# Optimization experiments

Measured on AMD Instinct MI355X. Metric: run time of the kernel, lower is better.

The kernel has to match this reference:

```python
import jax, jax.numpy as jnp
import numpy as np

B, S, D, H = 2, 2048, 1024, 16
DK = D // H
NEG = -1000000000.0


def setup_inputs() -> dict:
    key = jax.random.key(0)
    ks = jax.random.split(key, 12)
    s = 1.0 / np.sqrt(D)
    return {
        "Q": jax.random.normal(ks[0], (B, S, D), jnp.float32),
        "K": jax.random.normal(ks[1], (B, S, D), jnp.float32),
        "V": jax.random.normal(ks[2], (B, S, D), jnp.float32),
        "attn_mask": jnp.zeros((B, S, S), jnp.bool_),
        "WQ_w": jax.random.normal(ks[3], (D, D), jnp.float32) * s,
        "WQ_b": jnp.zeros((D,), jnp.float32),
        "WK_w": jax.random.normal(ks[4], (D, D), jnp.float32) * s,
        "WK_b": jnp.zeros((D,), jnp.float32),
        "WV_w": jax.random.normal(ks[5], (D, D), jnp.float32) * s,
        "WV_b": jnp.zeros((D,), jnp.float32),
        "fc_w": jax.random.normal(ks[6], (D, D), jnp.float32) * s,
        "fc_b": jnp.zeros((D,), jnp.float32),
    }


def reference(Q, K, V, attn_mask, WQ_w, WQ_b, WK_w, WK_b, WV_w, WV_b, fc_w, fc_b):
    b = Q.shape[0]
    # linear projections (torch Linear: x @ W^T + b), split heads -> [b, h, s, dk]
    q = (Q @ WQ_w.T + WQ_b).reshape(b, -1, H, DK).transpose(0, 2, 1, 3)
    k = (K @ WK_w.T + WK_b).reshape(b, -1, H, DK).transpose(0, 2, 1, 3)
    v = (V @ WV_w.T + WV_b).reshape(b, -1, H, DK).transpose(0, 2, 1, 3)
    # scaled dot-product attention with masked_fill
    scores = jnp.einsum("bhqd,bhkd->bhqk", q, k) / jnp.sqrt(jnp.float32(DK))
    scores = jnp.where(attn_mask[:, None, :, :], NEG, scores)
    attn_weights = jax.nn.softmax(scores, axis=-1)  # dropout p=0 -> identity
    attn = jnp.einsum("bhqk,bhkd->bhqd", attn_weights, v)
    attn = attn.transpose(0, 2, 1, 3).reshape(b, -1, H * DK)
    output = attn @ fc_w.T + fc_b
    return output, attn_weights
```

## Files before the change

### kernel.cpp

```cpp
#include <hip/hip_runtime.h>
#include <cstdint>
#include <cstddef>

constexpr int CB = 2;
constexpr int CS = 2048;
constexpr int CD = 1024;
constexpr int CH = 16;
constexpr int CDK = 64;
constexpr float NEGV = -1000000000.0f;

typedef __bf16 bf16x8 __attribute__((ext_vector_type(8)));
typedef float f32x4 __attribute__((ext_vector_type(4)));
typedef unsigned short u16x8 __attribute__((ext_vector_type(8)));
typedef unsigned short u16x4 __attribute__((ext_vector_type(4)));

static __device__ __forceinline__ unsigned short f2bf(float x) {
  unsigned int u = __float_as_uint(x);
  u += 0x7fffu + ((u >> 16) & 1u);
  return (unsigned short)(u >> 16);
}
static __device__ __forceinline__ bf16x8 bc8(u16x8 u) {
  return __builtin_bit_cast(bf16x8, u);
}
static __device__ __forceinline__ f32x4 mfma16(bf16x8 a, bf16x8 b, f32x4 c) {
  return __builtin_amdgcn_mfma_f32_16x16x32_bf16(a, b, c, 0, 0, 0);
}

struct CvtArgs {
  const float* src[7];
  unsigned short* dst[7];
  int n4[7];
};

__global__ __launch_bounds__(256) void cvt_all(CvtArgs a) {
  const int r = blockIdx.y;
  const float* __restrict__ in = a.src[r];
  unsigned short* __restrict__ out = a.dst[r];
  const int n4 = a.n4[r];
  const int stride = gridDim.x * 256;
  for (int i = blockIdx.x * 256 + threadIdx.x; i < n4; i += stride) {
    float4 v = reinterpret_cast<const float4*>(in)[i];
    u16x4 o;
    o[0] = f2bf(v.x); o[1] = f2bf(v.y); o[2] = f2bf(v.z); o[3] = f2bf(v.w);
    reinterpret_cast<u16x4*>(out)[i] = o;
  }
}

constexpr int GBM = 128, GBN = 64, GBK = 32, GLD = 40;

template <int MODE>
__global__ __launch_bounds__(256) void gemm_nt(const unsigned short* __restrict__ X,
                                               const unsigned short* __restrict__ Wt,
                                               const float* __restrict__ bias,
                                               void* __restrict__ outp,
                                               int M, int N, int K, float oscale) {
  __shared__ unsigned short lA[GBM * GLD];
  __shared__ unsigned short lB[GBN * GLD];
  const int tid = threadIdx.x, lane = tid & 63, wid = tid >> 6;
  const int mbase = blockIdx.y * GBM, nbase = blockIdx.x * GBN;
  const int wm = (wid & 1) * 64, wn = (wid >> 1) * 32;
  const int trow = tid >> 2, tcol = (tid & 3) * 8;

  f32x4 acc[4][2] = {};

  for (int k0 = 0; k0 < K; k0 += GBK) {
    __syncthreads();
    *reinterpret_cast<u16x8*>(&lA[trow * GLD + tcol]) =
        *reinterpret_cast<const u16x8*>(&X[(size_t)(mbase + trow) * K + k0 + tcol]);
    *reinterpret_cast<u16x8*>(&lA[(trow + 64) * GLD + tcol]) =
        *reinterpret_cast<const u16x8*>(&X[(size_t)(mbase + trow + 64) * K + k0 + tcol]);
    *reinterpret_cast<u16x8*>(&lB[trow * GLD + tcol]) =
        *reinterpret_cast<const u16x8*>(&Wt[(size_t)(nbase + trow) * K + k0 + tcol]);
    __syncthreads();

    bf16x8 af[4], bfv[2];
#pragma unroll
    for (int i = 0; i < 4; ++i)
      af[i] = bc8(*reinterpret_cast<const u16x8*>(
          &lA[(wm + i * 16 + (lane & 15)) * GLD + (lane >> 4) * 8]));
#pragma unroll
    for (int j = 0; j < 2; ++j)
      bfv[j] = bc8(*reinterpret_cast<const u16x8*>(
          &lB[(wn + j * 16 + (lane & 15)) * GLD + (lane >> 4) * 8]));
#pragma unroll
    for (int i = 0; i < 4; ++i)
#pragma unroll
      for (int j = 0; j < 2; ++j)
        acc[i][j] = mfma16(af[i], bfv[j], acc[i][j]);
  }

#pragma unroll
  for (int j = 0; j < 2; ++j) {
    const int colb = nbase + wn + j * 16 + (lane & 15);
    const float bv = bias[colb];
#pragma unroll
    for (int i = 0; i < 4; ++i) {
#pragma unroll
      for (int r = 0; r < 4; ++r) {
        const int rowb = mbase + wm + i * 16 + (lane >> 4) * 4 + r;
        const float v = (acc[i][j][r] + bv) * oscale;
        if constexpr (MODE == 2) {
          reinterpret_cast<float*>(outp)[(size_t)rowb * N + colb] = v;
        } else {
          const int bb = rowb >> 11, sr = rowb & (CS - 1);
          const int hh = colb >> 6, dk = colb & (CDK - 1);
          if constexpr (MODE == 0)
            reinterpret_cast<unsigned short*>(outp)[(((size_t)bb * CH + hh) * CS + sr) * CDK + dk] =
                f2bf(v);
          else
            reinterpret_cast<unsigned short*>(outp)[(((size_t)bb * CH + hh) * CDK + dk) * CS + sr] =
                f2bf(v);
        }
      }
    }
  }
}

constexpr int WLD = 68;

__global__ __launch_bounds__(256, 4) void attn_fused(const unsigned short* __restrict__ qh,
                                                     const unsigned short* __restrict__ kh,
                                                     const unsigned short* __restrict__ vT,
                                                     const unsigned char* __restrict__ mask,
                                                     float* __restrict__ attnw,
                                                     unsigned short* __restrict__ attn_pre) {
  __shared__ unsigned short lK[2][64 * 64];
  __shared__ float lW[4][16 * WLD];

  const int tid = threadIdx.x, lane = tid & 63, wid = tid >> 6;
  const int bid = blockIdx.x;
  const int swz = (bid & 7) * 128 + (bid >> 3);
  const int qt = swz & 31, hh = (swz >> 5) & 15, b = swz >> 9;
  const int bh = b * CH + hh;
  const int qw = qt * 64 + wid * 16;
  const int fr = lane & 15, fc = lane >> 4;

  const unsigned short* qp = qh + ((size_t)bh * CS + qw + fr) * CDK + fc * 8;
  const bf16x8 aq0 = bc8(*reinterpret_cast<const u16x8*>(qp));
  const bf16x8 aq1 = bc8(*reinterpret_cast<const u16x8*>(qp + 32));

  const char* ktile0 = (const char*)(kh + (size_t)bh * CS * CDK);
  const unsigned char* mrow = mask + ((size_t)b * CS + qw + (lane >> 2)) * CS + (lane & 3) * 16;

  auto stage = [&](int buf, int kt) {
    const char* src = ktile0 + (size_t)kt * 8192;
#pragma unroll
    for (int cc = 0; cc < 2; ++cc) {
      const int ob = (wid * 2 + cc) * 1024;
      const int o = ob + lane * 16;
      const int so = o ^ (((o >> 7) & 7) << 4);
      __builtin_amdgcn_global_load_lds(
          (const __attribute__((address_space(1))) void*)(src + so),
          (__attribute__((address_space(3))) void*)((char*)(&lK[buf][0]) + ob), 16, 0, 0);
    }
  };
  auto kfr = [&](int buf, int g, int half) -> bf16x8 {
    const int row = g * 16 + fr;
    const int slot = (fc + half * 4) ^ (row & 7);
    return bc8(*reinterpret_cast<const u16x8*>(&lK[buf][row * 64 + slot * 8]));
  };

  float l_r[4] = {0.f, 0.f, 0.f, 0.f};
  unsigned int dirtybits = 0;

  stage(0, 0);
  __syncthreads();
  for (int kt = 0; kt < CS / 64; ++kt) {
    if (kt < CS / 64 - 1) stage((kt + 1) & 1, kt + 1);
    const uint4 mv = *reinterpret_cast<const uint4*>(mrow + kt * 64);
    const int nz = (mv.x | mv.y | mv.z | mv.w) != 0;
    const int dirty = __ballot(nz) != 0ull;
    const int buf = kt & 1;

    f32x4 sf[4];
#pragma unroll
    for (int g = 0; g < 4; ++g) {
      f32x4 a = {0.f, 0.f, 0.f, 0.f};
      a = mfma16(aq0, kfr(buf, g, 0), a);
      a = mfma16(aq1, kfr(buf, g, 1), a);
      sf[g] = a;
    }
    if (dirty) {
      dirtybits |= (1u << kt);
#pragma unroll
      for (int g = 0; g < 4; ++g)
#pragma unroll
        for (int r = 0; r < 4; ++r) {
          const unsigned char mb =
              mask[((size_t)b * CS + qw + fc * 4 + r) * CS + kt * 64 + g * 16 + fr];
          if (mb) sf[g][r] = NEGV;
        }
    }
#pragma unroll
    for (int r = 0; r < 4; ++r)
      l_r[r] += __expf(sf[0][r]) + __expf(sf[1][r]) + __expf(sf[2][r]) + __expf(sf[3][r]);
    __syncthreads();
  }

  float linv[4];
#pragma unroll
  for (int r = 0; r < 4; ++r) {
    float s = l_r[r];
    s += __shfl_xor(s, 1);
    s += __shfl_xor(s, 2);
    s += __shfl_xor(s, 4);
    s += __shfl_xor(s, 8);
    linv[r] = 1.0f / s;
  }

  const unsigned short* vfrag = vT + ((size_t)bh * CDK + fr) * CS + fc * 8;

  f32x4 o[4] = {};
  stage(0, 0);
  __syncthreads();
  for (int kt = 0; kt < CS / 64; ++kt) {
    if (kt < CS / 64 - 1) stage((kt + 1) & 1, kt + 1);
    const int buf = kt & 1;

    u16x8 vr[8];
#pragma unroll
    for (int g = 0; g < 4; ++g) {
      const unsigned short* vp = vfrag + (size_t)g * 16 * CS + kt * 64;
      vr[2 * g] = *reinterpret_cast<const u16x8*>(vp);
      vr[2 * g + 1] = *reinterpret_cast<const u16x8*>(vp + 32);
    }

    f32x4 sf[4];
#pragma unroll
    for (int g = 0; g < 4; ++g) {
      f32x4 a = {0.f, 0.f, 0.f, 0.f};
      a = mfma16(aq0, kfr(buf, g, 0), a);
      a = mfma16(aq1, kfr(buf, g, 1), a);
      sf[g] = a;
    }
    if ((dirtybits >> kt) & 1u) {
#pragma unroll
      for (int g = 0; g < 4; ++g)
#pragma unroll
        for (int r = 0; r < 4; ++r) {
          const unsigned char mb =
              mask[((size_t)b * CS + qw + fc * 4 + r) * CS + kt * 64 + g * 16 + fr];
          if (mb) sf[g][r] = NEGV;
        }
    }
#pragma unroll
    for (int g = 0; g < 4; ++g)
#pragma unroll
      for (int r = 0; r < 4; ++r) sf[g][r] = __expf(sf[g][r]) * linv[r];

#pragma unroll
    for (int g = 0; g < 4; ++g)
#pragma unroll
      for (int r = 0; r < 4; ++r)
        lW[wid][(fc * 4 + r) * WLD + g * 16 + fr] = sf[g][r];

#pragma unroll
    for (int it = 0; it < 4; ++it) {
      const int row = it * 4 + fc;
      const f32x4 wv = *reinterpret_cast<const f32x4*>(&lW[wid][row * WLD + fr * 4]);
      __builtin_nontemporal_store(
          wv, reinterpret_cast<f32x4*>(
                  &attnw[((size_t)bh * CS + qw + row) * CS + kt * 64 + fr * 4]));
    }

    bf16x8 wa[2];
#pragma unroll
    for (int c = 0; c < 2; ++c) {
      const f32x4 t0 = *reinterpret_cast<const f32x4*>(&lW[wid][fr * WLD + c * 32 + fc * 8]);
      const f32x4 t1 = *reinterpret_cast<const f32x4*>(&lW[wid][fr * WLD + c * 32 + fc * 8 + 4]);
      u16x8 u;
#pragma unroll
      for (int z = 0; z < 4; ++z) { u[z] = f2bf(t0[z]); u[z + 4] = f2bf(t1[z]); }
      wa[c] = bc8(u);
    }
#pragma unroll
    for (int g = 0; g < 4; ++g) {
      o[g] = mfma16(wa[0], bc8(vr[2 * g]), o[g]);
      o[g] = mfma16(wa[1], bc8(vr[2 * g + 1]), o[g]);
    }
    __syncthreads();
  }

#pragma unroll
  for (int g = 0; g < 4; ++g)
#pragma unroll
    for (int r = 0; r < 4; ++r) {
      const int q = qw + fc * 4 + r;
      attn_pre[(((size_t)b * CS + q) * CH + hh) * CDK + g * 16 + fr] = f2bf(o[g][r]);
    }
}

extern "C" void kernel_launch(void* const* d_in, const int* in_sizes, int n_in,
                              void* d_out, int out_size, void* d_ws, size_t ws_size,
                              hipStream_t stream) {
  (void)in_sizes; (void)n_in; (void)out_size; (void)ws_size;

  const float* Qf = (const float*)d_in[0];
  const float* Kf = (const float*)d_in[1];
  const float* Vf = (const float*)d_in[2];
  const unsigned char* mask = (const unsigned char*)d_in[3];
  const float* WQw = (const float*)d_in[4];
  const float* WQb = (const float*)d_in[5];
  const float* WKw = (const float*)d_in[6];
  const float* WKb = (const float*)d_in[7];
  const float* WVw = (const float*)d_in[8];
  const float* WVb = (const float*)d_in[9];
  const float* fcw = (const float*)d_in[10];
  const float* fcb = (const float*)d_in[11];

  float* out0 = (float*)d_out;
  float* attnw = out0 + (size_t)CB * CS * CD;

  char* w = (char*)d_ws;
  unsigned short* Qb = (unsigned short*)(w);
  unsigned short* Kb = (unsigned short*)(w + 8388608);
  unsigned short* Vb = (unsigned short*)(w + 2 * 8388608);
  unsigned short* Wqb = (unsigned short*)(w + 3 * 8388608);
  unsigned short* Wkb = Wqb + 1048576;
  unsigned short* Wvb = Wkb + 1048576;
  unsigned short* Wfb = Wvb + 1048576;
  unsigned short* qhp = (unsigned short*)(w + 3 * 8388608 + 4 * 2097152);
  unsigned short* khp = qhp + 4194304;
  unsigned short* vTp = khp + 4194304;
  unsigned short* apre = Qb;

  const int NELEM4 = (CB * CS * CD) / 4;
  const int WELEM4 = (CD * CD) / 4;

  CvtArgs ca;
  ca.src[0] = Qf;  ca.dst[0] = Qb;  ca.n4[0] = NELEM4;
  ca.src[1] = Kf;  ca.dst[1] = Kb;  ca.n4[1] = NELEM4;
  ca.src[2] = Vf;  ca.dst[2] = Vb;  ca.n4[2] = NELEM4;
  ca.src[3] = WQw; ca.dst[3] = Wqb; ca.n4[3] = WELEM4;
  ca.src[4] = WKw; ca.dst[4] = Wkb; ca.n4[4] = WELEM4;
  ca.src[5] = WVw; ca.dst[5] = Wvb; ca.n4[5] = WELEM4;
  ca.src[6] = fcw; ca.dst[6] = Wfb; ca.n4[6] = WELEM4;
  cvt_all<<<dim3(512, 7), 256, 0, stream>>>(ca);

  dim3 gg(CD / GBN, (CB * CS) / GBM);
  gemm_nt<0><<<gg, 256, 0, stream>>>(Qb, Wqb, WQb, qhp, CB * CS, CD, CD, 0.125f);
  gemm_nt<0><<<gg, 256, 0, stream>>>(Kb, Wkb, WKb, khp, CB * CS, CD, CD, 1.0f);
  gemm_nt<1><<<gg, 256, 0, stream>>>(Vb, Wvb, WVb, vTp, CB * CS, CD, CD, 1.0f);

  attn_fused<<<dim3(1024), 256, 0, stream>>>(qhp, khp, vTp, mask, attnw, apre);

  gemm_nt<2><<<gg, 256, 0, stream>>>(apre, Wfb, fcb, out0, CB * CS, CD, CD, 1.0f);
}
```

Before: 293.0 us.

## Pre-swizzle K/V into MFMA fragment layout, batch QKV GEMMs, drop LDS staging

The QKV projections now run as one batched launch, and the GEMM body uses async global-to-LDS loads with double buffering and an XOR swizzle. The K and V projections are written straight into a per-tile MFMA fragment layout, so the attention kernel loads K and V fragments directly into registers. This removes the K shared-memory staging and the per-tile barriers. The Q scale folds in log2(e) so softmax can use exp2f, mask dirtiness is precomputed in a prologue, and P is converted to bf16 with the packed cvt instruction. Occupancy hint drops to 3 blocks per SM, trading register pressure for the register-held K/V prefetch.

After: 257.2 us. 1.14x faster.

```diff
diff --git a/kernel.cpp b/kernel.cpp
--- a/kernel.cpp
+++ b/kernel.cpp
@@ -8,6 +8,7 @@
 constexpr int CH = 16;
 constexpr int CDK = 64;
 constexpr float NEGV = -1000000000.0f;
+constexpr float QSCALE = 0.18033688011112042f;
 
 typedef __bf16 bf16x8 __attribute__((ext_vector_type(8)));
 typedef float f32x4 __attribute__((ext_vector_type(4)));
@@ -46,85 +47,124 @@
   }
 }
 
-constexpr int GBM = 128, GBN = 64, GBK = 32, GLD = 40;
-
-template <int MODE>
-__global__ __launch_bounds__(256) void gemm_nt(const unsigned short* __restrict__ X,
+constexpr int GK = 1024, GNT = GK / 32;
+
+struct QKVArgs {
+  const unsigned short* X[3];
+  const unsigned short* W[3];
+  const float* bias[3];
+  unsigned short* out[3];
+  float osc[3];
+};
+
+template <typename EPI>
+__device__ __forceinline__ void gemm_body(const unsigned short* __restrict__ X,
+                                          const unsigned short* __restrict__ Wt,
+                                          EPI epi) {
+  __shared__ unsigned short lA[2][128 * 32];
+  __shared__ unsigned short lB[2][64 * 32];
+  const int tid = threadIdx.x, lane = tid & 63, wid = tid >> 6;
+  const int fr = lane & 15, fc = lane >> 4;
+  const int mbase = blockIdx.y * 128, nbase = blockIdx.x * 64;
+  const int wm = (wid & 1) * 64, wn = (wid >> 1) * 32;
+
+  const int srow = wid * 16 + (lane >> 2);
+  const int sslot = (lane & 3) ^ (srow & 3);
+  const unsigned short* a0 = X + (size_t)(mbase + srow) * GK + sslot * 8;
+  const unsigned short* b0 = Wt + (size_t)(nbase + srow) * GK + sslot * 8;
+
+  auto stage = [&](int buf, int k0) {
+    __builtin_amdgcn_global_load_lds(
+        (const __attribute__((address_space(1))) void*)(a0 + k0),
+        (__attribute__((address_space(3))) void*)((char*)&lA[buf][0] + wid * 1024), 16, 0, 0);
+    __builtin_amdgcn_global_load_lds(
+        (const __attribute__((address_space(1))) void*)(a0 + (size_t)64 * GK + k0),
+        (__attribute__((address_space(3))) void*)((char*)&lA[buf][0] + 4096 + wid * 1024), 16, 0, 0);
+    __builtin_amdgcn_global_load_lds(
+        (const __attribute__((address_space(1))) void*)(b0 + k0),
+        (__attribute__((address_space(3))) void*)((char*)&lB[buf][0] + wid * 1024), 16, 0, 0);
+  };
+
+  f32x4 acc[4][2] = {};
+  stage(0, 0);
+  __syncthreads();
+  for (int t = 0; t < GNT; ++t) {
+    if (t + 1 < GNT) stage((t + 1) & 1, (t + 1) * 32);
+    const int buf = t & 1;
+    bf16x8 af[4], bfv[2];
+#pragma unroll
+    for (int i = 0; i < 4; ++i) {
+      const int row = wm + i * 16 + fr;
+      af[i] = bc8(*reinterpret_cast<const u16x8*>(&lA[buf][row * 32 + ((fc ^ (row & 3)) * 8)]));
+    }
+#pragma unroll
+    for (int j = 0; j < 2; ++j) {
+      const int row = wn + j * 16 + fr;
+      bfv[j] = bc8(*reinterpret_cast<const u16x8*>(&lB[buf][row * 32 + ((fc ^ (row & 3)) * 8)]));
+    }
+#pragma unroll
+    for (int i = 0; i < 4; ++i)
+#pragma unroll
+      for (int j = 0; j < 2; ++j)
+        acc[i][j] = mfma16(af[i], bfv[j], acc[i][j]);
+    __syncthreads();
+  }
+
+#pragma unroll
+  for (int j = 0; j < 2; ++j) {
+    const int colb = nbase + wn + j * 16 + fr;
+#pragma unroll
+    for (int i = 0; i < 4; ++i) {
+#pragma unroll
+      for (int r = 0; r < 4; ++r) {
+        const int rowb = mbase + wm + i * 16 + fc * 4 + r;
+        epi(rowb, colb, acc[i][j][r]);
+      }
+    }
+  }
+}
+
+__global__ __launch_bounds__(256) void gemm_qkv(QKVArgs a) {
+  const int z = blockIdx.z;
+  const float* bias = a.bias[z];
+  unsigned short* out = a.out[z];
+  const float osc = a.osc[z];
+  gemm_body(a.X[z], a.W[z], [&](int rowb, int colb, float av) {
+    const float v = (av + bias[colb]) * osc;
+    const int bb = rowb >> 11, sr = rowb & (CS - 1);
+    const int hh = colb >> 6, cc = colb & (CDK - 1);
+    const size_t bh = (size_t)bb * CH + hh;
+    if (z == 0) {
+      out[(bh * CS + sr) * CDK + cc] = f2bf(v);
+    } else if (z == 1) {
+      const int kt = sr >> 6, ww = sr & 63, g = ww >> 4, fr2 = ww & 15;
+      const int half = cc >> 5, fc2 = (cc >> 3) & 3, zz = cc & 7;
+      out[(bh * 256 + kt * 8 + g * 2 + half) * 512 + (fc2 * 16 + fr2) * 8 + zz] = f2bf(v);
+    } else {
+      const int kt = sr >> 6, ww = sr & 63, c2 = ww >> 5, fc2 = (ww >> 3) & 3, zz = ww & 7;
+      const int g = cc >> 4, fr2 = cc & 15;
+      out[(bh * 256 + kt * 8 + g * 2 + c2) * 512 + (fc2 * 16 + fr2) * 8 + zz] = f2bf(v);
+    }
+  });
+}
+
+__global__ __launch_bounds__(256) void gemm_fc(const unsigned short* __restrict__ X,
                                                const unsigned short* __restrict__ Wt,
                                                const float* __restrict__ bias,
-                                               void* __restrict__ outp,
-                                               int M, int N, int K, float oscale) {
-  __shared__ unsigned short lA[GBM * GLD];
-  __shared__ unsigned short lB[GBN * GLD];
-  const int tid = threadIdx.x, lane = tid & 63, wid = tid >> 6;
-  const int mbase = blockIdx.y * GBM, nbase = blockIdx.x * GBN;
-  const int wm = (wid & 1) * 64, wn = (wid >> 1) * 32;
-  const int trow = tid >> 2, tcol = (tid & 3) * 8;
-
-  f32x4 acc[4][2] = {};
-
-  for (int k0 = 0; k0 < K; k0 += GBK) {
-    __syncthreads();
-    *reinterpret_cast<u16x8*>(&lA[trow * GLD + tcol]) =
-        *reinterpret_cast<const u16x8*>(&X[(size_t)(mbase + trow) * K + k0 + tcol]);
-    *reinterpret_cast<u16x8*>(&lA[(trow + 64) * GLD + tcol]) =
-        *reinterpret_cast<const u16x8*>(&X[(size_t)(mbase + trow + 64) * K + k0 + tcol]);
-    *reinterpret_cast<u16x8*>(&lB[trow * GLD + tcol]) =
-        *reinterpret_cast<const u16x8*>(&Wt[(size_t)(nbase + trow) * K + k0 + tcol]);
-    __syncthreads();
-
-    bf16x8 af[4], bfv[2];
-#pragma unroll
-    for (int i = 0; i < 4; ++i)
-      af[i] = bc8(*reinterpret_cast<const u16x8*>(
-          &lA[(wm + i * 16 + (lane & 15)) * GLD + (lane >> 4) * 8]));
-#pragma unroll
-    for (int j = 0; j < 2; ++j)
-      bfv[j] = bc8(*reinterpret_cast<const u16x8*>(
-          &lB[(wn + j * 16 + (lane & 15)) * GLD + (lane >> 4) * 8]));
-#pragma unroll
-    for (int i = 0; i < 4; ++i)
-#pragma unroll
-      for (int j = 0; j < 2; ++j)
-        acc[i][j] = mfma16(af[i], bfv[j], acc[i][j]);
-  }
-
-#pragma unroll
-  for (int j = 0; j < 2; ++j) {
-    const int colb = nbase + wn + j * 16 + (lane & 15);
-    const float bv = bias[colb];
-#pragma unroll
-    for (int i = 0; i < 4; ++i) {
-#pragma unroll
-      for (int r = 0; r < 4; ++r) {
-        const int rowb = mbase + wm + i * 16 + (lane >> 4) * 4 + r;
-        const float v = (acc[i][j][r] + bv) * oscale;
-        if constexpr (MODE == 2) {
-          reinterpret_cast<float*>(outp)[(size_t)rowb * N + colb] = v;
-        } else {
-          const int bb = rowb >> 11, sr = rowb & (CS - 1);
-          const int hh = colb >> 6, dk = colb & (CDK - 1);
-          if constexpr (MODE == 0)
-            reinterpret_cast<unsigned short*>(outp)[(((size_t)bb * CH + hh) * CS + sr) * CDK + dk] =
-                f2bf(v);
-          else
-            reinterpret_cast<unsigned short*>(outp)[(((size_t)bb * CH + hh) * CDK + dk) * CS + sr] =
-                f2bf(v);
-        }
-      }
-    }
-  }
+                                               float* __restrict__ out) {
+  gemm_body(X, Wt, [&](int rowb, int colb, float av) {
+    out[(size_t)rowb * CD + colb] = av + bias[colb];
+  });
 }
 
 constexpr int WLD = 68;
 
-__global__ __launch_bounds__(256, 4) void attn_fused(const unsigned short* __restrict__ qh,
-                                                     const unsigned short* __restrict__ kh,
+__global__ __launch_bounds__(256, 3) void attn_fused(const unsigned short* __restrict__ qh,
+                                                     const unsigned short* __restrict__ kT,
                                                      const unsigned short* __restrict__ vT,
                                                      const unsigned char* __restrict__ mask,
                                                      float* __restrict__ attnw,
                                                      unsigned short* __restrict__ attn_pre) {
-  __shared__ unsigned short lK[2][64 * 64];
   __shared__ float lW[4][16 * WLD];
 
   const int tid = threadIdx.x, lane = tid & 63, wid = tid >> 6;
@@ -139,62 +179,50 @@
   const bf16x8 aq0 = bc8(*reinterpret_cast<const u16x8*>(qp));
   const bf16x8 aq1 = bc8(*reinterpret_cast<const u16x8*>(qp + 32));
 
-  const char* ktile0 = (const char*)(kh + (size_t)bh * CS * CDK);
+  const unsigned short* kbase = kT + (size_t)bh * 131072 + lane * 8;
+  const unsigned short* vbase = vT + (size_t)bh * 131072 + lane * 8;
+
   const unsigned char* mrow = mask + ((size_t)b * CS + qw + (lane >> 2)) * CS + (lane & 3) * 16;
-
-  auto stage = [&](int buf, int kt) {
-    const char* src = ktile0 + (size_t)kt * 8192;
-#pragma unroll
-    for (int cc = 0; cc < 2; ++cc) {
-      const int ob = (wid * 2 + cc) * 1024;
-      const int o = ob + lane * 16;
-      const int so = o ^ (((o >> 7) & 7) << 4);
-      __builtin_amdgcn_global_load_lds(
-          (const __attribute__((address_space(1))) void*)(src + so),
-          (__attribute__((address_space(3))) void*)((char*)(&lK[buf][0]) + ob), 16, 0, 0);
-    }
+  unsigned int dirtybits = 0;
+#pragma unroll 4
+  for (int kt = 0; kt < 32; ++kt) {
+    const uint4 mv = *reinterpret_cast<const uint4*>(mrow + kt * 64);
+    if (__ballot((mv.x | mv.y | mv.z | mv.w) != 0)) dirtybits |= (1u << kt);
+  }
+
+  u16x8 kreg[8];
+  auto loadK = [&](int kt) {
+    const unsigned short* p = kbase + (size_t)kt * 4096;
+#pragma unroll
+    for (int f = 0; f < 8; ++f) kreg[f] = *reinterpret_cast<const u16x8*>(p + f * 512);
   };
-  auto kfr = [&](int buf, int g, int half) -> bf16x8 {
-    const int row = g * 16 + fr;
-    const int slot = (fc + half * 4) ^ (row & 7);
-    return bc8(*reinterpret_cast<const u16x8*>(&lK[buf][row * 64 + slot * 8]));
+  auto maskfix = [&](f32x4 (&sf)[4], int kt) {
+#pragma unroll
+    for (int g = 0; g < 4; ++g)
+#pragma unroll
+      for (int r = 0; r < 4; ++r) {
+        const unsigned char mb =
+            mask[((size_t)b * CS + qw + fc * 4 + r) * CS + kt * 64 + g * 16 + fr];
+        if (mb) sf[g][r] = NEGV;
+      }
   };
 
   float l_r[4] = {0.f, 0.f, 0.f, 0.f};
-  unsigned int dirtybits = 0;
-
-  stage(0, 0);
-  __syncthreads();
-  for (int kt = 0; kt < CS / 64; ++kt) {
-    if (kt < CS / 64 - 1) stage((kt + 1) & 1, kt + 1);
-    const uint4 mv = *reinterpret_cast<const uint4*>(mrow + kt * 64);
-    const int nz = (mv.x | mv.y | mv.z | mv.w) != 0;
-    const int dirty = __ballot(nz) != 0ull;
-    const int buf = kt & 1;
-
+  loadK(0);
+  for (int kt = 0; kt < 32; ++kt) {
     f32x4 sf[4];
 #pragma unroll
     for (int g = 0; g < 4; ++g) {
       f32x4 a = {0.f, 0.f, 0.f, 0.f};
-      a = mfma16(aq0, kfr(buf, g, 0), a);
-      a = mfma16(aq1, kfr(buf, g, 1), a);
+      a = mfma16(aq0, bc8(kreg[2 * g]), a);
+      a = mfma16(aq1, bc8(kreg[2 * g + 1]), a);
       sf[g] = a;
     }
-    if (dirty) {
-      dirtybits |= (1u << kt);
-#pragma unroll
-      for (int g = 0; g < 4; ++g)
-#pragma unroll
-        for (int r = 0; r < 4; ++r) {
-          const unsigned char mb =
-              mask[((size_t)b * CS + qw + fc * 4 + r) * CS + kt * 64 + g * 16 + fr];
-          if (mb) sf[g][r] = NEGV;
-        }
-    }
+    loadK(kt + 1 < 32 ? kt + 1 : 0);
+    if ((dirtybits >> kt) & 1u) maskfix(sf, kt);
 #pragma unroll
     for (int r = 0; r < 4; ++r)
-      l_r[r] += __expf(sf[0][r]) + __expf(sf[1][r]) + __expf(sf[2][r]) + __expf(sf[3][r]);
-    __syncthreads();
+      l_r[r] += exp2f(sf[0][r]) + exp2f(sf[1][r]) + exp2f(sf[2][r]) + exp2f(sf[3][r]);
   }
 
   float linv[4];
@@ -208,45 +236,32 @@
     linv[r] = 1.0f / s;
   }
 
-  const unsigned short* vfrag = vT + ((size_t)bh * CDK + fr) * CS + fc * 8;
-
   f32x4 o[4] = {};
-  stage(0, 0);
-  __syncthreads();
-  for (int kt = 0; kt < CS / 64; ++kt) {
-    if (kt < CS / 64 - 1) stage((kt + 1) & 1, kt + 1);
-    const int buf = kt & 1;
-
-    u16x8 vr[8];
-#pragma unroll
-    for (int g = 0; g < 4; ++g) {
-      const unsigned short* vp = vfrag + (size_t)g * 16 * CS + kt * 64;
-      vr[2 * g] = *reinterpret_cast<const u16x8*>(vp);
-      vr[2 * g + 1] = *reinterpret_cast<const u16x8*>(vp + 32);
-    }
+  u16x8 vreg[8];
+  auto loadV = [&](int kt) {
+    const unsigned short* p = vbase + (size_t)kt * 4096;
+#pragma unroll
+    for (int f = 0; f < 8; ++f) vreg[f] = *reinterpret_cast<const u16x8*>(p + f * 512);
+  };
+  loadK(0);
+  for (int kt = 0; kt < 32; ++kt) {
+    loadV(kt);
 
     f32x4 sf[4];
 #pragma unroll
     for (int g = 0; g < 4; ++g) {
       f32x4 a = {0.f, 0.f, 0.f, 0.f};
-      a = mfma16(aq0, kfr(buf, g, 0), a);
-      a = mfma16(aq1, kfr(buf, g, 1), a);
+      a = mfma16(aq0, bc8(kreg[2 * g]), a);
+      a = mfma16(aq1, bc8(kreg[2 * g + 1]), a);
       sf[g] = a;
     }
-    if ((dirtybits >> kt) & 1u) {
-#pragma unroll
-      for (int g = 0; g < 4; ++g)
-#pragma unroll
-        for (int r = 0; r < 4; ++r) {
-          const unsigned char mb =
-              mask[((size_t)b * CS + qw + fc * 4 + r) * CS + kt * 64 + g * 16 + fr];
-          if (mb) sf[g][r] = NEGV;
-        }
-    }
+    loadK(kt + 1 < 32 ? kt + 1 : 0);
+    if ((dirtybits >> kt) & 1u) maskfix(sf, kt);
+
 #pragma unroll
     for (int g = 0; g < 4; ++g)
 #pragma unroll
-      for (int r = 0; r < 4; ++r) sf[g][r] = __expf(sf[g][r]) * linv[r];
+      for (int r = 0; r < 4; ++r) sf[g][r] = exp2f(sf[g][r]) * linv[r];
 
 #pragma unroll
     for (int g = 0; g < 4; ++g)
@@ -268,17 +283,19 @@
     for (int c = 0; c < 2; ++c) {
       const f32x4 t0 = *reinterpret_cast<const f32x4*>(&lW[wid][fr * WLD + c * 32 + fc * 8]);
       const f32x4 t1 = *reinterpret_cast<const f32x4*>(&lW[wid][fr * WLD + c * 32 + fc * 8 + 4]);
-      u16x8 u;
-#pragma unroll
-      for (int z = 0; z < 4; ++z) { u[z] = f2bf(t0[z]); u[z + 4] = f2bf(t1[z]); }
-      wa[c] = bc8(u);
+      unsigned int w0, w1, w2, w3;
+      asm("v_cvt_pk_bf16_f32 %0, %1, %2" : "=v"(w0) : "v"(t0[0]), "v"(t0[1]));
+      asm("v_cvt_pk_bf16_f32 %0, %1, %2" : "=v"(w1) : "v"(t0[2]), "v"(t0[3]));
+      asm("v_cvt_pk_bf16_f32 %0, %1, %2" : "=v"(w2) : "v"(t1[0]), "v"(t1[1]));
+      asm("v_cvt_pk_bf16_f32 %0, %1, %2" : "=v"(w3) : "v"(t1[2]), "v"(t1[3]));
+      uint4 uw = {w0, w1, w2, w3};
+      wa[c] = __builtin_bit_cast(bf16x8, uw);
     }
 #pragma unroll
     for (int g = 0; g < 4; ++g) {
-      o[g] = mfma16(wa[0], bc8(vr[2 * g]), o[g]);
-      o[g] = mfma16(wa[1], bc8(vr[2 * g + 1]), o[g]);
-    }
-    __syncthreads();
+      o[g] = mfma16(wa[0], bc8(vreg[2 * g]), o[g]);
+      o[g] = mfma16(wa[1], bc8(vreg[2 * g + 1]), o[g]);
+    }
   }
 
 #pragma unroll
@@ -320,8 +337,8 @@
   unsigned short* Wvb = Wkb + 1048576;
   unsigned short* Wfb = Wvb + 1048576;
   unsigned short* qhp = (unsigned short*)(w + 3 * 8388608 + 4 * 2097152);
-  unsigned short* khp = qhp + 4194304;
-  unsigned short* vTp = khp + 4194304;
+  unsigned short* kTp = qhp + 4194304;
+  unsigned short* vTp = kTp + 4194304;
   unsigned short* apre = Qb;
 
   const int NELEM4 = (CB * CS * CD) / 4;
@@ -337,12 +354,13 @@
   ca.src[6] = fcw; ca.dst[6] = Wfb; ca.n4[6] = WELEM4;
   cvt_all<<<dim3(512, 7), 256, 0, stream>>>(ca);
 
-  dim3 gg(CD / GBN, (CB * CS) / GBM);
-  gemm_nt<0><<<gg, 256, 0, stream>>>(Qb, Wqb, WQb, qhp, CB * CS, CD, CD, 0.125f);
-  gemm_nt<0><<<gg, 256, 0, stream>>>(Kb, Wkb, WKb, khp, CB * CS, CD, CD, 1.0f);
-  gemm_nt<1><<<gg, 256, 0, stream>>>(Vb, Wvb, WVb, vTp, CB * CS, CD, CD, 1.0f);
-
-  attn_fused<<<dim3(1024), 256, 0, stream>>>(qhp, khp, vTp, mask, attnw, apre);
-
-  gemm_nt<2><<<gg, 256, 0, stream>>>(apre, Wfb, fcb, out0, CB * CS, CD, CD, 1.0f);
-}
+  QKVArgs qa;
+  qa.X[0] = Qb;  qa.W[0] = Wqb; qa.bias[0] = WQb; qa.out[0] = qhp; qa.osc[0] = QSCALE;
+  qa.X[1] = Kb;  qa.W[1] = Wkb; qa.bias[1] = WKb; qa.out[1] = kTp; qa.osc[1] = 1.0f;
+  qa.X[2] = Vb;  qa.W[2] = Wvb; qa.bias[2] = WVb; qa.out[2] = vTp; qa.osc[2] = 1.0f;
+  gemm_qkv<<<dim3(CD / 64, (CB * CS) / 128, 3), 256, 0, stream>>>(qa);
+
+  attn_fused<<<dim3(1024), 256, 0, stream>>>(qhp, kTp, vTp, mask, attnw, apre);
+
+  gemm_fc<<<dim3(CD / 64, (CB * CS) / 128), 256, 0, stream>>>(apre, Wfb, fcb, out0);
+}
```
